# Optimization experiments

Measured on AMD Instinct MI355X. Metric: run time of the kernel, lower is better.

Reference implementation:

```python
import math
import jax, jax.numpy as jnp
import numpy as np

EPS = 1e-7
MAX_TANH_ARG = 1.0 - 1e-5

def _norm(x):
    return jnp.sqrt(jnp.sum(x * x, axis=-1, keepdims=True)).clip(EPS)

def logmap0(x):  # Poincare ball, c=1
    n = _norm(x)
    return jnp.arctanh(jnp.clip(n, EPS, MAX_TANH_ARG)) * x / n

def expmap0(v):
    n = _norm(v)
    return jnp.tanh(n) * v / n

def mobius_add(x, y):
    x2 = jnp.sum(x * x, -1, keepdims=True)
    y2 = jnp.sum(y * y, -1, keepdims=True)
    xy = jnp.sum(x * y, -1, keepdims=True)
    num = (1 + 2 * xy + y2) * x + (1 - x2) * y
    den = (1 + 2 * xy + x2 * y2).clip(EPS)
    return num / den

def plin(x, w, b):  # PoincareLinear: tangent-space affine map
    return expmap0(logmap0(x) @ w + b)

def layer_norm(x, eps=1e-6):  # elementwise_affine=False
    m = x.mean(-1, keepdims=True)
    v = ((x - m) ** 2).mean(-1, keepdims=True)
    return (x - m) / jnp.sqrt(v + eps)

def _beta(a, b):
    return math.exp(math.lgamma(a) + math.lgamma(b) - math.lgamma(a + b))

D, H, FF = 1024, 16, 4096
HD = D // H
BETA_N = _beta(D / 2, 0.5)   # beta(n/2, 1/2) for full dim
BETA_H = _beta(HD / 2, 0.5)  # beta(ni/2, 1/2) for head dim


def setup_inputs() -> dict:
    key = jax.random.key(0)
    ks = jax.random.split(key, 20)
    B, S = 4, 1024
    x = expmap0(0.02 * jax.random.normal(ks[0], (B, S, D), jnp.float32))
    t_emb = jax.random.normal(ks[1], (B, 1, D), jnp.float32)
    g = lambda k, sh: 0.02 * jax.random.normal(k, sh, jnp.float32)
    return {
        'x': x, 't_emb': t_emb,
        'w_q': g(ks[2], (D, D)), 'b_q': jnp.zeros((D,), jnp.float32),
        'w_k': g(ks[3], (D, D)), 'b_k': jnp.zeros((D,), jnp.float32),
        'w_v': g(ks[4], (D, D)), 'b_v': jnp.zeros((D,), jnp.float32),
        'w_o': g(ks[5], (D, D)), 'b_o': jnp.zeros((D,), jnp.float32),
        'w_f1': g(ks[6], (D, FF)), 'b_f1': jnp.zeros((FF,), jnp.float32),
        'w_f2': g(ks[7], (FF, D)), 'b_f2': jnp.zeros((D,), jnp.float32),
        'w_ada': g(ks[8], (D, 6 * D)), 'b_ada': jnp.zeros((6 * D,), jnp.float32),
    }


def _to_heads(p):
    # beta-split: logmap0, split per head, scale by beta_ni/beta_n, expmap0
    B, S, _ = p.shape
    t = logmap0(p).reshape(B, S, H, HD) * (BETA_H / BETA_N)
    return expmap0(jnp.transpose(t, (0, 2, 1, 3)))  # [B,H,S,HD]


def _from_heads(ph):
    # beta-concat: logmap0 per head, scale by beta_n/beta_ni, concat, expmap0
    B, _, S, _ = ph.shape
    t = logmap0(ph) * (BETA_N / BETA_H)
    t = jnp.transpose(t, (0, 2, 1, 3)).reshape(B, S, D)
    return expmap0(t)


def reference(x, t_emb, w_q, b_q, w_k, b_k, w_v, b_v, w_o, b_o,
              w_f1, b_f1, w_f2, b_f2, w_ada, b_ada):
    ada = t_emb @ w_ada + b_ada  # [B,1,6D]
    sh_msa, sc_msa, g_msa, sh_mlp, sc_mlp, g_mlp = jnp.split(ada, 6, axis=-1)

    # --- attention block ---
    residual = x
    xn = layer_norm(logmap0(x))
    xm = expmap0(xn * (1 + sc_msa) + sh_msa)

    q = _to_heads(plin(xm, w_q, b_q))
    k = _to_heads(plin(xm, w_k, b_k))
    v = _to_heads(plin(xm, w_v, b_v))

    qt, kt, vt = logmap0(q), logmap0(k), logmap0(v)
    scores = jnp.einsum('bhqd,bhkd->bhqk', qt, kt) / math.sqrt(HD)
    attn = jax.nn.softmax(scores, axis=-1)
    out_h = expmap0(jnp.einsum('bhqk,bhkd->bhqd', attn, vt))  # [B,H,S,HD]

    attn_out = plin(_from_heads(out_h), w_o, b_o)
    attn_t = g_msa * logmap0(attn_out)
    x = mobius_add(residual, expmap0(attn_t))

    # --- FFN block ---
    residual = x
    xn = layer_norm(logmap0(x))
    xm = expmap0(xn * (1 + sc_mlp) + sh_mlp)
    ff = plin(plin(xm, w_f1, b_f1), w_f2, b_f2)
    ff_t = g_mlp * logmap0(ff)
    return mobius_add(residual, expmap0(ff_t))
```

## Files before the change

### kernel.cpp

```cpp
#include <hip/hip_runtime.h>
#include <cmath>


constexpr int kD  = 1024;
constexpr int kH  = 16;
constexpr int kHD = 64;
constexpr int kFF = 4096;
constexpr int kB  = 4;
constexpr int kS  = 1024;
constexpr int kN  = kB * kS;

#define EPSF 1e-7f
#define MTAF (1.0f - 1e-5f)
#define LOG2E 1.4426950408889634f

typedef unsigned int uint32;
typedef unsigned short ushort16;
typedef __attribute__((ext_vector_type(8))) short short8x;
typedef __attribute__((ext_vector_type(4))) float floatx4;

__device__ __forceinline__ ushort16 f2b(float f) {
  union { float f; uint32 u; } x; x.f = f;
  uint32 r = x.u + 0x7fffu + ((x.u >> 16) & 1u);
  return (ushort16)(r >> 16);
}
__device__ __forceinline__ float b2f(ushort16 u) {
  union { uint32 u; float f; } x; x.u = ((uint32)u) << 16;
  return x.f;
}
__device__ __forceinline__ void load_b4(const ushort16* p, float v[4]) {
  uint2 u = *(const uint2*)p;
  v[0] = b2f((ushort16)(u.x & 0xffff)); v[1] = b2f((ushort16)(u.x >> 16));
  v[2] = b2f((ushort16)(u.y & 0xffff)); v[3] = b2f((ushort16)(u.y >> 16));
}
__device__ __forceinline__ void store_b4(ushort16* p, const float v[4]) {
  uint2 u;
  u.x = (uint32)f2b(v[0]) | ((uint32)f2b(v[1]) << 16);
  u.y = (uint32)f2b(v[2]) | ((uint32)f2b(v[3]) << 16);
  *(uint2*)p = u;
}

__device__ __forceinline__ float atanh_clipped(float n) {
  float c = fminf(n, MTAF);
  return 0.5f * logf((1.0f + c) / (1.0f - c));
}
__device__ __forceinline__ float logmap0_scale(float nraw) {
  float n = fmaxf(nraw, EPSF);
  return atanh_clipped(n) / n;
}
__device__ __forceinline__ float expmap0_scale(float nraw) {
  float n = fmaxf(nraw, EPSF);
  return tanhf(n) / n;
}
__device__ __forceinline__ float roundtrip_scale(float nraw) {
  float nu = fmaxf(nraw, EPSF);
  float se = tanhf(nu) / nu;
  float nb = fmaxf(se * nraw, EPSF);
  float sl = atanh_clipped(nb) / nb;
  return sl * se;
}

__device__ __forceinline__ float blockReduceSum256(float v, float* s4) {
#pragma unroll
  for (int o = 32; o > 0; o >>= 1) v += __shfl_xor(v, o);
  int wave = threadIdx.x >> 6;
  if ((threadIdx.x & 63) == 0) s4[wave] = v;
  __syncthreads();
  float r = s4[0] + s4[1] + s4[2] + s4[3];
  __syncthreads();
  return r;
}
__device__ __forceinline__ float redSum16(float v) {
#pragma unroll
  for (int o = 8; o > 0; o >>= 1) v += __shfl_xor(v, o);
  return v;
}

__device__ __forceinline__ void async16(const void* g, void* l) {
  __builtin_amdgcn_global_load_lds(
      (const __attribute__((address_space(1))) uint32*)g,
      (__attribute__((address_space(3))) uint32*)l, 16, 0, 0);
}

__device__ __forceinline__ void transpose_tile(const float* __restrict__ src,
                                               ushort16* __restrict__ dst,
                                               int K, int N, int n0, int k0) {
  __shared__ float T[64][65];
  int tid = threadIdx.x;
#pragma unroll
  for (int p = 0; p < 4; ++p) {
    int idx = p * 1024 + tid * 4;
    int r = idx >> 6, c = idx & 63;
    float4 t = *(const float4*)&src[(size_t)(k0 + r) * N + n0 + c];
    T[r][c] = t.x; T[r][c + 1] = t.y; T[r][c + 2] = t.z; T[r][c + 3] = t.w;
  }
  __syncthreads();
#pragma unroll
  for (int p = 0; p < 4; ++p) {
    int idx = p * 1024 + tid * 4;
    int r = idx >> 6, c = idx & 63;
    float v[4] = {T[c][r], T[c + 1][r], T[c + 2][r], T[c + 3][r]};
    store_b4(&dst[(size_t)(n0 + r) * K + k0 + c], v);
  }
}
__global__ __launch_bounds__(256) void k_transpose_bf16(const float* __restrict__ src,
                                                        ushort16* __restrict__ dst,
                                                        int K, int N) {
  transpose_tile(src, dst, K, N, blockIdx.x * 64, blockIdx.y * 64);
}
__global__ __launch_bounds__(256) void k_transpose4(
    const float* __restrict__ s0, const float* __restrict__ s1,
    const float* __restrict__ s2, const float* __restrict__ s3,
    ushort16* __restrict__ d0, ushort16* __restrict__ d1,
    ushort16* __restrict__ d2, ushort16* __restrict__ d3) {
  const float* src = (blockIdx.z == 0) ? s0 : (blockIdx.z == 1) ? s1
                    : (blockIdx.z == 2) ? s2 : s3;
  ushort16* dst = (blockIdx.z == 0) ? d0 : (blockIdx.z == 1) ? d1
                 : (blockIdx.z == 2) ? d2 : d3;
  transpose_tile(src, dst, kD, kD, blockIdx.x * 64, blockIdx.y * 64);
}

__global__ __launch_bounds__(256) void k_ada(const float* __restrict__ t_emb,
                                             const float* __restrict__ w_ada,
                                             const float* __restrict__ b_ada,
                                             float* __restrict__ ada) {
  __shared__ float te[kD];
  __shared__ float part[4][64];
  int b = blockIdx.y;
  int tid = threadIdx.x;
  {
    float4 t = *(const float4*)&t_emb[b * kD + tid * 4];
    te[tid * 4] = t.x; te[tid * 4 + 1] = t.y; te[tid * 4 + 2] = t.z; te[tid * 4 + 3] = t.w;
  }
  __syncthreads();
  int c = tid & 63, kc = tid >> 6;
  int col = blockIdx.x * 64 + c;
  float acc = 0.f;
#pragma unroll 8
  for (int k = kc * 256; k < kc * 256 + 256; ++k)
    acc += te[k] * w_ada[(size_t)k * (6 * kD) + col];
  part[kc][c] = acc;
  __syncthreads();
  if (tid < 64)
    ada[b * 6 * kD + blockIdx.x * 64 + tid] =
        part[0][tid] + part[1][tid] + part[2][tid] + part[3][tid] +
        b_ada[blockIdx.x * 64 + tid];
}

__global__ __launch_bounds__(256) void k_prenorm(const float* __restrict__ x,
                                                 const float* __restrict__ ada,
                                                 int sh_off, int sc_off,
                                                 ushort16* __restrict__ out) {
  __shared__ float sred[4];
  int tok = blockIdx.x;
  int b = tok >> 10;
  int d4 = threadIdx.x * 4;
  float xv[4];
  *(float4*)xv = *(const float4*)&x[(size_t)tok * kD + d4];
  float ss = xv[0] * xv[0] + xv[1] * xv[1] + xv[2] * xv[2] + xv[3] * xv[3];
  ss = blockReduceSum256(ss, sred);
  float sl = logmap0_scale(sqrtf(ss));
  float sum = 0.f;
#pragma unroll
  for (int i = 0; i < 4; ++i) { xv[i] *= sl; sum += xv[i]; }
  sum = blockReduceSum256(sum, sred);
  float mean = sum * (1.0f / kD);
  float vs = 0.f;
#pragma unroll
  for (int i = 0; i < 4; ++i) { xv[i] -= mean; vs += xv[i] * xv[i]; }
  vs = blockReduceSum256(vs, sred);
  float inv = rsqrtf(vs * (1.0f / kD) + 1e-6f);
  float shv[4], scv[4];
  *(float4*)shv = *(const float4*)&ada[b * 6 * kD + sh_off + d4];
  *(float4*)scv = *(const float4*)&ada[b * 6 * kD + sc_off + d4];
  float uu = 0.f;
#pragma unroll
  for (int i = 0; i < 4; ++i) {
    float u = xv[i] * inv * (1.0f + scv[i]) + shv[i];
    xv[i] = u;
    uu += u * u;
  }
  uu = blockReduceSum256(uu, sred);
  float s = roundtrip_scale(sqrtf(uu));
#pragma unroll
  for (int i = 0; i < 4; ++i) xv[i] *= s;
  store_b4(out + (size_t)tok * kD + d4, xv);
}

template <int OUT_BF16, int KSPLIT>
__global__ __launch_bounds__(512, 2) void k_gemm_bf16(
    const ushort16* __restrict__ A,
    const ushort16* __restrict__ Bt0, const ushort16* __restrict__ Bt1,
    const ushort16* __restrict__ Bt2,
    const float* __restrict__ bias0, const float* __restrict__ bias1,
    const float* __restrict__ bias2,
    const float* __restrict__ rowscale,
    void* __restrict__ C0, void* __restrict__ C1, void* __restrict__ C2,
    int M, int N, int K) {
  const ushort16* Bt;
  const float* bias;
  void* C;
  int k_lo, k_hi;
  bool add_bias;
  if (KSPLIT == 1) {
    Bt = (blockIdx.z == 0) ? Bt0 : ((blockIdx.z == 1) ? Bt1 : Bt2);
    bias = (blockIdx.z == 0) ? bias0 : ((blockIdx.z == 1) ? bias1 : bias2);
    C = (blockIdx.z == 0) ? C0 : ((blockIdx.z == 1) ? C1 : C2);
    k_lo = 0; k_hi = K; add_bias = true;
  } else {
    Bt = Bt0; bias = bias0;
    C = (blockIdx.z == 0) ? C0 : C1;
    int kchunk = K / KSPLIT;
    k_lo = blockIdx.z * kchunk; k_hi = k_lo + kchunk;
    add_bias = (blockIdx.z == 0);
  }

  __shared__ __align__(16) ushort16 As[2 * 256 * 64];
  __shared__ __align__(16) ushort16 Bs[2 * 128 * 64];

  int tid = threadIdx.x;
  int lane = tid & 63;
  int wave = tid >> 6;
  int wr = wave >> 1, wc = wave & 1;
  int c16 = lane & 15, quad = lane >> 4;
  int row0 = blockIdx.x * 256, col0 = blockIdx.y * 128;

  int srow = tid >> 3;
  int scol = (((tid & 7) ^ ((tid >> 4) & 7)) << 3);
  const ushort16* a_src = A + (size_t)(row0 + srow) * K + k_lo + scol;
  const ushort16* b_src = Bt + (size_t)(col0 + srow) * K + k_lo + scol;
  int sdst = tid * 8;
  int nt = (k_hi - k_lo) >> 6;

  auto stage = [&](int tt) {
    int cc = tt & 1;
    size_t ko = (size_t)tt * 64;
#pragma unroll
    for (int p = 0; p < 4; ++p)
      async16(a_src + ko + (size_t)(p * 64) * K, (ushort16*)As + cc * 16384 + p * 4096 + sdst);
#pragma unroll
    for (int p = 0; p < 2; ++p)
      async16(b_src + ko + (size_t)(p * 64) * K, (ushort16*)Bs + cc * 8192 + p * 4096 + sdst);
  };

  int xsw = (c16 >> 1) & 7;
  int aoff0 = (wr * 64 + c16) * 64 + ((quad ^ xsw) << 3);
  int aoff1 = (wr * 64 + c16) * 64 + (((4 + quad) ^ xsw) << 3);
  int boff0 = (wc * 64 + c16) * 64 + ((quad ^ xsw) << 3);
  int boff1 = (wc * 64 + c16) * 64 + (((4 + quad) ^ xsw) << 3);

  floatx4 acc[4][4];
#pragma unroll
  for (int i = 0; i < 4; ++i)
#pragma unroll
    for (int j = 0; j < 4; ++j) acc[i][j] = (floatx4)0.f;

  stage(0);
  stage(1);
  asm volatile("s_waitcnt vmcnt(6)" ::: "memory");
  __builtin_amdgcn_s_barrier();

  for (int t = 0; t < nt; ++t) {
    int cc = t & 1;
    const ushort16* Ab = (const ushort16*)As + cc * 16384;
    const ushort16* Bb = (const ushort16*)Bs + cc * 8192;
    short8x a[4][2], b[4][2];
#pragma unroll
    for (int i = 0; i < 4; ++i) {
      a[i][0] = *(const short8x*)&Ab[i * 1024 + aoff0];
      a[i][1] = *(const short8x*)&Ab[i * 1024 + aoff1];
      b[i][0] = *(const short8x*)&Bb[i * 1024 + boff0];
      b[i][1] = *(const short8x*)&Bb[i * 1024 + boff1];
    }
    __builtin_amdgcn_s_setprio(1);
#pragma unroll
    for (int i = 0; i < 4; ++i)
#pragma unroll
      for (int j = 0; j < 4; ++j)
        acc[i][j] = __builtin_amdgcn_mfma_f32_16x16x32_bf16(a[i][0], b[j][0], acc[i][j], 0, 0, 0);
    __builtin_amdgcn_s_setprio(0);
    asm volatile("s_waitcnt lgkmcnt(0)" ::: "memory");
    __builtin_amdgcn_s_barrier();
    if (t + 2 < nt) stage(t + 2);
    __builtin_amdgcn_s_setprio(1);
#pragma unroll
    for (int i = 0; i < 4; ++i)
#pragma unroll
      for (int j = 0; j < 4; ++j)
        acc[i][j] = __builtin_amdgcn_mfma_f32_16x16x32_bf16(a[i][1], b[j][1], acc[i][j], 0, 0, 0);
    __builtin_amdgcn_s_setprio(0);
    if (t + 2 < nt) {
      asm volatile("s_waitcnt vmcnt(6)" ::: "memory");
    } else {
      asm volatile("s_waitcnt vmcnt(0)" ::: "memory");
    }
    __builtin_amdgcn_s_barrier();
  }

  float bv[4];
#pragma unroll
  for (int j = 0; j < 4; ++j)
    bv[j] = add_bias ? bias[col0 + wc * 64 + j * 16 + c16] : 0.f;
  int rowq = quad * 4;
#pragma unroll
  for (int i = 0; i < 4; ++i) {
    int rbase = row0 + wr * 64 + i * 16 + rowq;
    float rs4[4];
#pragma unroll
    for (int r = 0; r < 4; ++r) rs4[r] = rowscale ? rowscale[rbase + r] : 1.0f;
#pragma unroll
    for (int j = 0; j < 4; ++j) {
      int c = col0 + wc * 64 + j * 16 + c16;
#pragma unroll
      for (int r = 0; r < 4; ++r) {
        float v = acc[i][j][r] * rs4[r] + bv[j];
        if (KSPLIT == 2) {
          if (blockIdx.z == 0) ((float*)C)[(size_t)(rbase + r) * N + c] = v;
          else ((ushort16*)C)[(size_t)(rbase + r) * N + c] = f2b(v);
        } else if (OUT_BF16) {
          ((ushort16*)C)[(size_t)(rbase + r) * N + c] = f2b(v);
        } else {
          ((float*)C)[(size_t)(rbase + r) * N + c] = v;
        }
      }
    }
  }
}

__global__ __launch_bounds__(256) void k_headsplit_b(const ushort16* __restrict__ q_in,
                                                     ushort16* __restrict__ k_io,
                                                     ushort16* __restrict__ v_io,
                                                     ushort16* __restrict__ qb_out,
                                                     float ratio) {
  __shared__ float sred[4];
  int tok = blockIdx.x;
  int tid = threadIdx.x;
  int d4 = tid * 4;
#pragma unroll
  for (int t = 0; t < 3; ++t) {
    const ushort16* p = (t == 0 ? q_in : (t == 1 ? (const ushort16*)k_io
                                                 : (const ushort16*)v_io)) +
                        (size_t)tok * kD + d4;
    float val[4];
    load_b4(p, val);
    float psq = val[0] * val[0] + val[1] * val[1] + val[2] * val[2] + val[3] * val[3];
    float hsq = redSum16(psq);
    float tot = blockReduceSum256(psq, sred);
    float s1 = roundtrip_scale(sqrtf(tot));
    float c = s1 * ratio;
    float s2 = roundtrip_scale(c * sqrtf(hsq));
    float f = c * s2 * (t == 0 ? (0.125f * LOG2E) : 1.0f);
#pragma unroll
    for (int i = 0; i < 4; ++i) val[i] *= f;
    ushort16* op = (t == 0 ? qb_out : (t == 1 ? k_io : v_io)) + (size_t)tok * kD + d4;
    store_b4(op, val);
    __syncthreads();
  }
}

__global__ __launch_bounds__(256) void k_vtrans_b(const ushort16* __restrict__ v,
                                                  ushort16* __restrict__ vT) {
  __shared__ ushort16 T[64][68];
  int bh = blockIdx.y, b = bh >> 4, h = bh & 15;
  int s0 = blockIdx.x * 64;
  int tid = threadIdx.x;
#pragma unroll
  for (int p = 0; p < 4; ++p) {
    int idx = p * 1024 + tid * 4;
    int r = idx >> 6, d = idx & 63;
    *(uint2*)&T[r][d] = *(const uint2*)&v[(size_t)(b * kS + s0 + r) * kD + h * kHD + d];
  }
  __syncthreads();
#pragma unroll
  for (int p = 0; p < 16; ++p) {
    int idx = p * 256 + tid;
    int d = idx >> 6, c = idx & 63;
    int cp = (c & 32) | ((c & 15) << 1) | ((c >> 4) & 1);
    vT[((size_t)bh * kHD + d) * kS + s0 + cp] = T[c][d];
  }
}

__global__ __launch_bounds__(256) void k_attn_mfma(ushort16* __restrict__ qb,
                                                   const ushort16* __restrict__ kb,
                                                   const ushort16* __restrict__ vT,
                                                   float ratio2) {
  __shared__ __align__(16) ushort16 Ks[2 * 128 * 32];
  __shared__ __align__(16) ushort16 Vs[4 * 64 * 32];
  __shared__ __align__(16) ushort16 Ps[4 * 4 * 16 * 40];
  int bh = blockIdx.x, b = bh >> 4, h = bh & 15;
  int q0 = blockIdx.y * 128;
  int tid = threadIdx.x, lane = tid & 63, wave = tid >> 6;
  int c16 = lane & 15, quad = lane >> 4;
  int sw = (lane >> 1) & 3;
  int cbp = ((quad ^ sw) << 3);
  int wq = wave * 32;

  short8x a_q[2][2];
#pragma unroll
  for (int i = 0; i < 2; ++i)
#pragma unroll
    for (int kk = 0; kk < 2; ++kk)
      a_q[i][kk] = *(const short8x*)&qb[(size_t)(b * kS + q0 + wq + i * 16 + c16) * kD +
                                        h * kHD + kk * 32 + quad * 8];

  short8x ones;
#pragma unroll
  for (int j = 0; j < 8; ++j) ones[j] = (short)0x3F80;

  floatx4 o[2][4], ol[2];
#pragma unroll
  for (int i = 0; i < 2; ++i) {
    ol[i] = (floatx4)0.f;
#pragma unroll
    for (int n = 0; n < 4; ++n) o[i][n] = (floatx4)0.f;
  }

  const ushort16* kbase = kb + ((size_t)b * kS) * kD + h * kHD;
  const ushort16* vbase = vT + (size_t)bh * kHD * kS;

  for (int k0 = 0; k0 < kS; k0 += 128) {
#pragma unroll
    for (int t = 0; t < 2; ++t)
#pragma unroll
      for (int cb2 = 0; cb2 < 2; ++cb2) {
        int e = cb2 * 2048 + tid * 8;
        int key = e >> 5;
        int col = ((((e >> 3) & 3) ^ ((key >> 1) & 3)) << 3);
        async16(kbase + (size_t)(k0 + key) * kD + t * 32 + col, Ks + t * 4096 + e);
      }
#pragma unroll
    for (int t = 0; t < 4; ++t) {
      int e = tid * 8;
      int dd = e >> 5;
      int col = ((((e >> 3) & 3) ^ ((dd >> 1) & 3)) << 3);
      async16(vbase + (size_t)dd * kS + k0 + t * 32 + col, Vs + t * 2048 + e);
    }
    __syncthreads();

#pragma unroll
    for (int i = 0; i < 2; ++i) {
      floatx4 s[8];
#pragma unroll
      for (int n = 0; n < 8; ++n) s[n] = (floatx4)0.f;
#pragma unroll
      for (int kkd = 0; kkd < 2; ++kkd)
#pragma unroll
        for (int n = 0; n < 8; ++n) {
          short8x bk = *(const short8x*)&Ks[kkd * 4096 + (n * 16 + c16) * 32 + cbp];
          s[n] = __builtin_amdgcn_mfma_f32_16x16x32_bf16(a_q[i][kkd], bk, s[n], 0, 0, 0);
        }

#pragma unroll
      for (int r = 0; r < 4; ++r) {
#pragma unroll
        for (int j = 0; j < 4; ++j) {
          uint32 u0 = (uint32)f2b(exp2f(s[2 * j][r]));
          uint32 u1 = (uint32)f2b(exp2f(s[2 * j + 1][r]));
          *(uint32*)&Ps[(((wave * 4 + j) * 16) + (quad * 4 + r)) * 40 + c16 * 2] =
              u0 | (u1 << 16);
        }
      }

#pragma unroll
      for (int kk = 0; kk < 4; ++kk) {
        short8x ap = *(const short8x*)&Ps[(((wave * 4 + kk) * 16) + c16) * 40 + quad * 8];
#pragma unroll
        for (int n = 0; n < 4; ++n) {
          short8x bv = *(const short8x*)&Vs[kk * 2048 + (n * 16 + c16) * 32 + cbp];
          o[i][n] = __builtin_amdgcn_mfma_f32_16x16x32_bf16(ap, bv, o[i][n], 0, 0, 0);
        }
        ol[i] = __builtin_amdgcn_mfma_f32_16x16x32_bf16(ap, ones, ol[i], 0, 0, 0);
      }
    }
    __syncthreads();
  }

#pragma unroll
  for (int i = 0; i < 2; ++i)
#pragma unroll
    for (int r = 0; r < 4; ++r) {
      float invl = 1.0f / ol[i][r];
      float w[4];
      float pssq = 0.f;
#pragma unroll
      for (int n = 0; n < 4; ++n) { w[n] = o[i][n][r] * invl; pssq += w[n] * w[n]; }
      float ssq = redSum16(pssq);
      float coef = roundtrip_scale(sqrtf(ssq)) * ratio2;
      int row = b * kS + q0 + wq + i * 16 + quad * 4 + r;
#pragma unroll
      for (int n = 0; n < 4; ++n)
        qb[(size_t)row * kD + h * kHD + n * 16 + c16] = f2b(coef * w[n]);
    }
}

template <int WIDTH>
__global__ __launch_bounds__(256) void k_rowscale(const ushort16* __restrict__ p,
                                                  float* __restrict__ s) {
  __shared__ float sred[4];
  constexpr int PER = WIDTH / 1024;
  size_t base = (size_t)blockIdx.x * WIDTH;
  float ss = 0.f;
#pragma unroll
  for (int i = 0; i < PER; ++i) {
    float v[4];
    load_b4(p + base + i * 1024 + threadIdx.x * 4, v);
    ss += v[0] * v[0] + v[1] * v[1] + v[2] * v[2] + v[3] * v[3];
  }
  ss = blockReduceSum256(ss, sred);
  if (threadIdx.x == 0) s[blockIdx.x] = roundtrip_scale(sqrtf(ss));
}

__device__ __forceinline__ void mobius_body(float xv[4], float tv[4],
                                            const float* gp, int d4,
                                            float* sred, float outv[4]) {
  float ss = tv[0] * tv[0] + tv[1] * tv[1] + tv[2] * tv[2] + tv[3] * tv[3];
  ss = blockReduceSum256(ss, sred);
  float s5 = roundtrip_scale(sqrtf(ss));
  float gv[4];
  *(float4*)gv = *(const float4*)&gp[d4];
  float at2 = 0.f;
#pragma unroll
  for (int i = 0; i < 4; ++i) {
    float a = gv[i] * s5 * tv[i];
    tv[i] = a;
    at2 += a * a;
  }
  at2 = blockReduceSum256(at2, sred);
  float nyraw = sqrtf(at2);
  float sy = expmap0_scale(nyraw);
  float ynorm = sy * nyraw;
  float y2 = ynorm * ynorm;
  float x2p = 0.f, xyp = 0.f;
#pragma unroll
  for (int i = 0; i < 4; ++i) {
    float y = sy * tv[i];
    tv[i] = y;
    x2p += xv[i] * xv[i];
    xyp += xv[i] * y;
  }
  float x2 = blockReduceSum256(x2p, sred);
  float xy = blockReduceSum256(xyp, sred);
  float cx = 1.0f + 2.0f * xy + y2;
  float cy = 1.0f - x2;
  float den = fmaxf(1.0f + 2.0f * xy + x2 * y2, EPSF);
  float invden = 1.0f / den;
#pragma unroll
  for (int i = 0; i < 4; ++i) outv[i] = (cx * xv[i] + cy * tv[i]) * invden;
}

__global__ __launch_bounds__(256) void k_epilogue2(const float* __restrict__ xres,
                                                   const float* __restrict__ ot0,
                                                   const ushort16* __restrict__ ot1b,
                                                   const float* __restrict__ ada,
                                                   int g_off,
                                                   float* __restrict__ out) {
  __shared__ float sred[4];
  int tok = blockIdx.x;
  int b = tok >> 10;
  size_t base = (size_t)tok * kD;
  int d4 = threadIdx.x * 4;
  float xv[4], tv[4], t1[4];
  *(float4*)tv = *(const float4*)&ot0[base + d4];
  load_b4(ot1b + base + d4, t1);
  *(float4*)xv = *(const float4*)&xres[base + d4];
#pragma unroll
  for (int i = 0; i < 4; ++i) tv[i] += t1[i];
  float outv[4];
  mobius_body(xv, tv, ada + b * 6 * kD + g_off, d4, sred, outv);
  *(float4*)&out[base + d4] = *(float4*)outv;
}

__global__ __launch_bounds__(256) void k_epi_pre(const float* __restrict__ xres,
                                                 const float* __restrict__ ot0,
                                                 const ushort16* __restrict__ ot1b,
                                                 const float* __restrict__ ada,
                                                 float* __restrict__ xmid_out,
                                                 ushort16* __restrict__ lx2_out) {
  __shared__ float sred[4];
  int tok = blockIdx.x;
  int b = tok >> 10;
  size_t base = (size_t)tok * kD;
  int d4 = threadIdx.x * 4;
  float xv[4], tv[4], t1[4];
  *(float4*)tv = *(const float4*)&ot0[base + d4];
  load_b4(ot1b + base + d4, t1);
  *(float4*)xv = *(const float4*)&xres[base + d4];
#pragma unroll
  for (int i = 0; i < 4; ++i) tv[i] += t1[i];
  float xm[4];
  mobius_body(xv, tv, ada + b * 6 * kD + 2 * kD, d4, sred, xm);
  *(float4*)&xmid_out[base + d4] = *(float4*)xm;

  float ss = xm[0] * xm[0] + xm[1] * xm[1] + xm[2] * xm[2] + xm[3] * xm[3];
  ss = blockReduceSum256(ss, sred);
  float sl = logmap0_scale(sqrtf(ss));
  float sum = 0.f;
#pragma unroll
  for (int i = 0; i < 4; ++i) { xm[i] *= sl; sum += xm[i]; }
  sum = blockReduceSum256(sum, sred);
  float mean = sum * (1.0f / kD);
  float vs = 0.f;
#pragma unroll
  for (int i = 0; i < 4; ++i) { xm[i] -= mean; vs += xm[i] * xm[i]; }
  vs = blockReduceSum256(vs, sred);
  float inv = rsqrtf(vs * (1.0f / kD) + 1e-6f);
  float shv[4], scv[4];
  *(float4*)shv = *(const float4*)&ada[b * 6 * kD + 3 * kD + d4];
  *(float4*)scv = *(const float4*)&ada[b * 6 * kD + 4 * kD + d4];
  float uu = 0.f;
#pragma unroll
  for (int i = 0; i < 4; ++i) {
    float u = xm[i] * inv * (1.0f + scv[i]) + shv[i];
    xm[i] = u;
    uu += u * u;
  }
  uu = blockReduceSum256(uu, sred);
  float s = roundtrip_scale(sqrtf(uu));
#pragma unroll
  for (int i = 0; i < 4; ++i) xm[i] *= s;
  store_b4(lx2_out + base + d4, xm);
}

extern "C" void kernel_launch(void* const* d_in, const int* in_sizes, int n_in,
                              void* d_out, int out_size, void* d_ws, size_t ws_size,
                              hipStream_t stream) {
  const float* x     = (const float*)d_in[0];
  const float* t_emb = (const float*)d_in[1];
  const float* w_q = (const float*)d_in[2];  const float* b_q = (const float*)d_in[3];
  const float* w_k = (const float*)d_in[4];  const float* b_k = (const float*)d_in[5];
  const float* w_v = (const float*)d_in[6];  const float* b_v = (const float*)d_in[7];
  const float* w_o = (const float*)d_in[8];  const float* b_o = (const float*)d_in[9];
  const float* w_f1 = (const float*)d_in[10]; const float* b_f1 = (const float*)d_in[11];
  const float* w_f2 = (const float*)d_in[12]; const float* b_f2 = (const float*)d_in[13];
  const float* w_ada = (const float*)d_in[14]; const float* b_ada = (const float*)d_in[15];
  float* out = (float*)d_out;

  constexpr size_t ND = (size_t)kN * kD;
  constexpr size_t NF = (size_t)kN * kFF;
  constexpr size_t DD = (size_t)kD * kD;

  float* ws   = (float*)d_ws;
  float* ada  = ws;
  float* qt   = ada + 6 * kD * kB;
  float* kt   = qt + ND;
  float* vt   = kt + ND;
  ushort16* qbA = (ushort16*)(vt + ND);
  ushort16* kb  = qbA + ND;
  ushort16* vTb = kb + ND;
  ushort16* actB = vTb + ND;
  ushort16* wqT  = actB + NF;
  ushort16* wkT  = wqT + DD;
  ushort16* wvT  = wkT + DD;
  ushort16* woT  = wvT + DD;
  ushort16* wf1T = woT + DD;
  ushort16* wf2T = wf1T + (size_t)kD * kFF;

  double bn = exp(lgamma(512.0) + lgamma(0.5) - lgamma(512.5));
  double bh = exp(lgamma(32.0) + lgamma(0.5) - lgamma(32.5));
  float R1 = (float)(bh / bn);
  float R2 = (float)(bn / bh);

  k_transpose4<<<dim3(16, 16, 4), 256, 0, stream>>>(w_q, w_k, w_v, w_o,
                                                    wqT, wkT, wvT, woT);
  k_transpose_bf16<<<dim3(64, 16), 256, 0, stream>>>(w_f1, wf1T, kD, kFF);
  k_transpose_bf16<<<dim3(16, 64), 256, 0, stream>>>(w_f2, wf2T, kFF, kD);
  k_ada<<<dim3(6 * kD / 64, kB), 256, 0, stream>>>(t_emb, w_ada, b_ada, ada);
  k_prenorm<<<kN, 256, 0, stream>>>(x, ada, 0 * kD, 1 * kD, qbA);
  k_gemm_bf16<1, 1><<<dim3(kN / 256, kD / 128, 3), 512, 0, stream>>>(
      qbA, wqT, wkT, wvT, b_q, b_k, b_v, nullptr, kb, vTb, actB, kN, kD, kD);
  k_headsplit_b<<<kN, 256, 0, stream>>>(kb, vTb, actB, qbA, R1);
  k_vtrans_b<<<dim3(kS / 64, kB * kH), 256, 0, stream>>>(actB, kb);
  k_attn_mfma<<<dim3(kB * kH, kS / 128), 256, 0, stream>>>(qbA, vTb, kb, R2);
  k_rowscale<kD><<<kN, 256, 0, stream>>>(qbA, kt);
  k_gemm_bf16<0, 2><<<dim3(kN / 256, kD / 128, 2), 512, 0, stream>>>(
      qbA, woT, woT, woT, b_o, b_o, b_o, kt, qt, kb, nullptr, kN, kD, kD);
  k_epi_pre<<<kN, 256, 0, stream>>>(x, qt, kb, ada, vt, qbA);
  k_gemm_bf16<1, 1><<<dim3(kN / 256, kFF / 128, 1), 512, 0, stream>>>(
      qbA, wf1T, wf1T, wf1T, b_f1, b_f1, b_f1, nullptr, actB, actB, actB, kN, kFF, kD);
  k_rowscale<kFF><<<kN, 256, 0, stream>>>(actB, kt);
  k_gemm_bf16<0, 2><<<dim3(kN / 256, kD / 128, 2), 512, 0, stream>>>(
      actB, wf2T, wf2T, wf2T, b_f2, b_f2, b_f2, kt, qt, kb, nullptr, kN, kD, kFF);
  k_epilogue2<<<kN, 256, 0, stream>>>(vt, qt, kb, ada, 5 * kD, out);

  (void)in_sizes; (void)n_in; (void)out_size; (void)ws_size;
}
```

Measured before the change: 432.5 us.

## Halve attention query tile per block, add MFMA priority hints and packed bf16 convert

The attention kernel now processes 64 query rows per block (16 per wave) instead of 128, doubling the grid to 1024 blocks so more workgroups are available to fill the CUs. MFMA sections are wrapped in s_setprio to favour matrix issue, and the per-element bf16 rounding is replaced with a single v_cvt_pk_bf16_f32 instruction. The cost is that each block now loads the K/V tiles for half as many queries, so total K/V global and LDS traffic doubles.

```diff
diff --git a/kernel.cpp b/kernel.cpp
--- a/kernel.cpp
+++ b/kernel.cpp
@@ -388,32 +388,27 @@
   __shared__ __align__(16) ushort16 Vs[4 * 64 * 32];
   __shared__ __align__(16) ushort16 Ps[4 * 4 * 16 * 40];
   int bh = blockIdx.x, b = bh >> 4, h = bh & 15;
-  int q0 = blockIdx.y * 128;
+  int q0 = blockIdx.y * 64;
   int tid = threadIdx.x, lane = tid & 63, wave = tid >> 6;
   int c16 = lane & 15, quad = lane >> 4;
   int sw = (lane >> 1) & 3;
   int cbp = ((quad ^ sw) << 3);
-  int wq = wave * 32;
-
-  short8x a_q[2][2];
-#pragma unroll
-  for (int i = 0; i < 2; ++i)
-#pragma unroll
-    for (int kk = 0; kk < 2; ++kk)
-      a_q[i][kk] = *(const short8x*)&qb[(size_t)(b * kS + q0 + wq + i * 16 + c16) * kD +
-                                        h * kHD + kk * 32 + quad * 8];
+  int wq = wave * 16;
+
+  short8x a_q[2];
+#pragma unroll
+  for (int kk = 0; kk < 2; ++kk)
+    a_q[kk] = *(const short8x*)&qb[(size_t)(b * kS + q0 + wq + c16) * kD +
+                                   h * kHD + kk * 32 + quad * 8];
 
   short8x ones;
 #pragma unroll
   for (int j = 0; j < 8; ++j) ones[j] = (short)0x3F80;
 
-  floatx4 o[2][4], ol[2];
-#pragma unroll
-  for (int i = 0; i < 2; ++i) {
-    ol[i] = (floatx4)0.f;
-#pragma unroll
-    for (int n = 0; n < 4; ++n) o[i][n] = (floatx4)0.f;
-  }
+  floatx4 o[4], ol;
+  ol = (floatx4)0.f;
+#pragma unroll
+  for (int n = 0; n < 4; ++n) o[n] = (floatx4)0.f;
 
   const ushort16* kbase = kb + ((size_t)b * kS) * kD + h * kHD;
   const ushort16* vbase = vT + (size_t)bh * kHD * kS;
@@ -437,60 +432,60 @@
     }
     __syncthreads();
 
-#pragma unroll
-    for (int i = 0; i < 2; ++i) {
-      floatx4 s[8];
-#pragma unroll
-      for (int n = 0; n < 8; ++n) s[n] = (floatx4)0.f;
-#pragma unroll
-      for (int kkd = 0; kkd < 2; ++kkd)
-#pragma unroll
-        for (int n = 0; n < 8; ++n) {
-          short8x bk = *(const short8x*)&Ks[kkd * 4096 + (n * 16 + c16) * 32 + cbp];
-          s[n] = __builtin_amdgcn_mfma_f32_16x16x32_bf16(a_q[i][kkd], bk, s[n], 0, 0, 0);
-        }
-
-#pragma unroll
-      for (int r = 0; r < 4; ++r) {
-#pragma unroll
-        for (int j = 0; j < 4; ++j) {
-          uint32 u0 = (uint32)f2b(exp2f(s[2 * j][r]));
-          uint32 u1 = (uint32)f2b(exp2f(s[2 * j + 1][r]));
-          *(uint32*)&Ps[(((wave * 4 + j) * 16) + (quad * 4 + r)) * 40 + c16 * 2] =
-              u0 | (u1 << 16);
-        }
+    floatx4 s[8];
+#pragma unroll
+    for (int n = 0; n < 8; ++n) s[n] = (floatx4)0.f;
+    __builtin_amdgcn_s_setprio(1);
+#pragma unroll
+    for (int kkd = 0; kkd < 2; ++kkd)
+#pragma unroll
+      for (int n = 0; n < 8; ++n) {
+        short8x bk = *(const short8x*)&Ks[kkd * 4096 + (n * 16 + c16) * 32 + cbp];
+        s[n] = __builtin_amdgcn_mfma_f32_16x16x32_bf16(a_q[kkd], bk, s[n], 0, 0, 0);
       }
-
-#pragma unroll
-      for (int kk = 0; kk < 4; ++kk) {
-        short8x ap = *(const short8x*)&Ps[(((wave * 4 + kk) * 16) + c16) * 40 + quad * 8];
-#pragma unroll
-        for (int n = 0; n < 4; ++n) {
-          short8x bv = *(const short8x*)&Vs[kk * 2048 + (n * 16 + c16) * 32 + cbp];
-          o[i][n] = __builtin_amdgcn_mfma_f32_16x16x32_bf16(ap, bv, o[i][n], 0, 0, 0);
-        }
-        ol[i] = __builtin_amdgcn_mfma_f32_16x16x32_bf16(ap, ones, ol[i], 0, 0, 0);
+    __builtin_amdgcn_s_setprio(0);
+
+#pragma unroll
+    for (int r = 0; r < 4; ++r) {
+#pragma unroll
+      for (int j = 0; j < 4; ++j) {
+        float e0 = exp2f(s[2 * j][r]);
+        float e1 = exp2f(s[2 * j + 1][r]);
+        uint32 u;
+        asm("v_cvt_pk_bf16_f32 %0, %1, %2" : "=v"(u) : "v"(e0), "v"(e1));
+        *(uint32*)&Ps[(((wave * 4 + j) * 16) + (quad * 4 + r)) * 40 + c16 * 2] = u;
       }
     }
+
+    __builtin_amdgcn_s_setprio(1);
+#pragma unroll
+    for (int kk = 0; kk < 4; ++kk) {
+      short8x ap = *(const short8x*)&Ps[(((wave * 4 + kk) * 16) + c16) * 40 + quad * 8];
+#pragma unroll
+      for (int n = 0; n < 4; ++n) {
+        short8x bv = *(const short8x*)&Vs[kk * 2048 + (n * 16 + c16) * 32 + cbp];
+        o[n] = __builtin_amdgcn_mfma_f32_16x16x32_bf16(ap, bv, o[n], 0, 0, 0);
+      }
+      ol = __builtin_amdgcn_mfma_f32_16x16x32_bf16(ap, ones, ol, 0, 0, 0);
+    }
+    __builtin_amdgcn_s_setprio(0);
     __syncthreads();
   }
 
 #pragma unroll
-  for (int i = 0; i < 2; ++i)
-#pragma unroll
-    for (int r = 0; r < 4; ++r) {
-      float invl = 1.0f / ol[i][r];
-      float w[4];
-      float pssq = 0.f;
-#pragma unroll
-      for (int n = 0; n < 4; ++n) { w[n] = o[i][n][r] * invl; pssq += w[n] * w[n]; }
-      float ssq = redSum16(pssq);
-      float coef = roundtrip_scale(sqrtf(ssq)) * ratio2;
-      int row = b * kS + q0 + wq + i * 16 + quad * 4 + r;
-#pragma unroll
-      for (int n = 0; n < 4; ++n)
-        qb[(size_t)row * kD + h * kHD + n * 16 + c16] = f2b(coef * w[n]);
-    }
+  for (int r = 0; r < 4; ++r) {
+    float invl = 1.0f / ol[r];
+    float w[4];
+    float pssq = 0.f;
+#pragma unroll
+    for (int n = 0; n < 4; ++n) { w[n] = o[n][r] * invl; pssq += w[n] * w[n]; }
+    float ssq = redSum16(pssq);
+    float coef = roundtrip_scale(sqrtf(ssq)) * ratio2;
+    int row = b * kS + q0 + wq + quad * 4 + r;
+#pragma unroll
+    for (int n = 0; n < 4; ++n)
+      qb[(size_t)row * kD + h * kHD + n * 16 + c16] = f2b(coef * w[n]);
+  }
 }
 
 template <int WIDTH>
@@ -670,7 +665,7 @@
       qbA, wqT, wkT, wvT, b_q, b_k, b_v, nullptr, kb, vTb, actB, kN, kD, kD);
   k_headsplit_b<<<kN, 256, 0, stream>>>(kb, vTb, actB, qbA, R1);
   k_vtrans_b<<<dim3(kS / 64, kB * kH), 256, 0, stream>>>(actB, kb);
-  k_attn_mfma<<<dim3(kB * kH, kS / 128), 256, 0, stream>>>(qbA, vTb, kb, R2);
+  k_attn_mfma<<<dim3(kB * kH, kS / 64), 256, 0, stream>>>(qbA, vTb, kb, R2);
   k_rowscale<kD><<<kN, 256, 0, stream>>>(qbA, kt);
   k_gemm_bf16<0, 2><<<dim3(kN / 256, kD / 128, 2), 512, 0, stream>>>(
       qbA, woT, woT, woT, b_o, b_o, b_o, kt, qt, kb, nullptr, kN, kD, kD);
```

New measurement: 430.6 us. No clear change (-0.5%).

## Double-buffer K tiles and overlap async loads with MFMA in attention kernel

Applied to the files above, without the earlier changes.

Makes the K shared-memory tile double-buffered and restructures the attention loop so the next V tile and the K tile two steps ahead are issued asynchronously while the current tile is computed. Explicit vmcnt waits and barriers replace the blocking syncthreads. It also raises wave priority around MFMA sections and converts exp values to bf16 with a packed conversion instruction. The intent is to hide global-load latency behind compute, at the cost of more shared memory per block and hand-counted waitcnt values that are easy to get wrong.

```diff
diff --git a/kernel.cpp b/kernel.cpp
--- a/kernel.cpp
+++ b/kernel.cpp
@@ -384,7 +384,7 @@
                                                    const ushort16* __restrict__ kb,
                                                    const ushort16* __restrict__ vT,
                                                    float ratio2) {
-  __shared__ __align__(16) ushort16 Ks[2 * 128 * 32];
+  __shared__ __align__(16) ushort16 Ks[2 * 2 * 128 * 32];
   __shared__ __align__(16) ushort16 Vs[4 * 64 * 32];
   __shared__ __align__(16) ushort16 Ps[4 * 4 * 16 * 40];
   int bh = blockIdx.x, b = bh >> 4, h = bh & 15;
@@ -394,6 +394,7 @@
   int sw = (lane >> 1) & 3;
   int cbp = ((quad ^ sw) << 3);
   int wq = wave * 32;
+  constexpr int NT = kS / 128;
 
   short8x a_q[2][2];
 #pragma unroll
@@ -418,49 +419,75 @@
   const ushort16* kbase = kb + ((size_t)b * kS) * kD + h * kHD;
   const ushort16* vbase = vT + (size_t)bh * kHD * kS;
 
-  for (int k0 = 0; k0 < kS; k0 += 128) {
-#pragma unroll
-    for (int t = 0; t < 2; ++t)
+  auto stageK = [&](int t) {
+    int cbuf = t & 1;
+#pragma unroll
+    for (int tt = 0; tt < 2; ++tt)
 #pragma unroll
       for (int cb2 = 0; cb2 < 2; ++cb2) {
         int e = cb2 * 2048 + tid * 8;
         int key = e >> 5;
         int col = ((((e >> 3) & 3) ^ ((key >> 1) & 3)) << 3);
-        async16(kbase + (size_t)(k0 + key) * kD + t * 32 + col, Ks + t * 4096 + e);
+        async16(kbase + (size_t)(t * 128 + key) * kD + tt * 32 + col,
+                Ks + cbuf * 8192 + tt * 4096 + e);
       }
-#pragma unroll
-    for (int t = 0; t < 4; ++t) {
+  };
+  auto stageV = [&](int t) {
+#pragma unroll
+    for (int tt = 0; tt < 4; ++tt) {
       int e = tid * 8;
       int dd = e >> 5;
       int col = ((((e >> 3) & 3) ^ ((dd >> 1) & 3)) << 3);
-      async16(vbase + (size_t)dd * kS + k0 + t * 32 + col, Vs + t * 2048 + e);
+      async16(vbase + (size_t)dd * kS + t * 128 + tt * 32 + col, Vs + tt * 2048 + e);
     }
-    __syncthreads();
+  };
+
+  stageK(0);
+  stageV(0);
+  stageK(1);
+  asm volatile("s_waitcnt vmcnt(8)" ::: "memory");
+  __builtin_amdgcn_s_barrier();
+
+  for (int t = 0; t < NT; ++t) {
+    const ushort16* Kc = (const ushort16*)Ks + (t & 1) * 8192;
 
 #pragma unroll
     for (int i = 0; i < 2; ++i) {
       floatx4 s[8];
 #pragma unroll
       for (int n = 0; n < 8; ++n) s[n] = (floatx4)0.f;
+      __builtin_amdgcn_s_setprio(1);
 #pragma unroll
       for (int kkd = 0; kkd < 2; ++kkd)
 #pragma unroll
         for (int n = 0; n < 8; ++n) {
-          short8x bk = *(const short8x*)&Ks[kkd * 4096 + (n * 16 + c16) * 32 + cbp];
+          short8x bk = *(const short8x*)&Kc[kkd * 4096 + (n * 16 + c16) * 32 + cbp];
           s[n] = __builtin_amdgcn_mfma_f32_16x16x32_bf16(a_q[i][kkd], bk, s[n], 0, 0, 0);
         }
+      __builtin_amdgcn_s_setprio(0);
 
 #pragma unroll
       for (int r = 0; r < 4; ++r) {
 #pragma unroll
         for (int j = 0; j < 4; ++j) {
-          uint32 u0 = (uint32)f2b(exp2f(s[2 * j][r]));
-          uint32 u1 = (uint32)f2b(exp2f(s[2 * j + 1][r]));
-          *(uint32*)&Ps[(((wave * 4 + j) * 16) + (quad * 4 + r)) * 40 + c16 * 2] =
-              u0 | (u1 << 16);
+          float e0 = exp2f(s[2 * j][r]);
+          float e1 = exp2f(s[2 * j + 1][r]);
+          uint32 u;
+          asm("v_cvt_pk_bf16_f32 %0, %1, %2" : "=v"(u) : "v"(e0), "v"(e1));
+          *(uint32*)&Ps[(((wave * 4 + j) * 16) + (quad * 4 + r)) * 40 + c16 * 2] = u;
         }
       }
 
+      if (i == 0) {
+        if (t + 1 < NT) {
+          asm volatile("s_waitcnt vmcnt(4)" ::: "memory");
+        } else {
+          asm volatile("s_waitcnt vmcnt(0)" ::: "memory");
+        }
+        __builtin_amdgcn_s_barrier();
+      }
+
+      __builtin_amdgcn_s_setprio(1);
 #pragma unroll
       for (int kk = 0; kk < 4; ++kk) {
         short8x ap = *(const short8x*)&Ps[(((wave * 4 + kk) * 16) + c16) * 40 + quad * 8];
@@ -471,8 +498,21 @@
         }
         ol[i] = __builtin_amdgcn_mfma_f32_16x16x32_bf16(ap, ones, ol[i], 0, 0, 0);
       }
+      __builtin_amdgcn_s_setprio(0);
     }
-    __syncthreads();
+
+    asm volatile("s_waitcnt lgkmcnt(0)" ::: "memory");
+    __builtin_amdgcn_s_barrier();
+    if (t + 1 < NT) stageV(t + 1);
+    if (t + 2 < NT) stageK(t + 2);
+    if (t + 2 < NT) {
+      asm volatile("s_waitcnt vmcnt(8)" ::: "memory");
+    } else if (t + 1 < NT) {
+      asm volatile("s_waitcnt vmcnt(4)" ::: "memory");
+    } else {
+      asm volatile("s_waitcnt vmcnt(0)" ::: "memory");
+    }
+    __builtin_amdgcn_s_barrier();
   }
 
 #pragma unroll
```

Result: no change. 427.9 us (-1.1%).
